# Optimization experiments

Hardware: AMD Instinct MI355X
Metric: run time of the kernel (lower is better)

Reference implementation:

```python
import jax, jax.numpy as jnp
import numpy as np
from jax import lax

C_OUT, C_IN, KH, KW = 16, 16, 3, 3
STRIDE = (1, 1)
PADDING = ((1, 1), (1, 1))  # symmetric 'same' padding for 3x3, stride 1
DILATION = (1, 1)


def setup_inputs() -> dict:
    key = jax.random.key(0)
    kx, kw = jax.random.split(key)
    x = jax.random.normal(kx, (8, C_IN, 512, 512), dtype=jnp.float32)
    # Conv2DUF stores the conv weight flattened: [out_channels, in_channels*kh*kw]
    weight = jax.random.normal(kw, (C_OUT, C_IN * KH * KW), dtype=jnp.float32) * 0.1
    return {"x": x, "weight": weight}


def reference(x, weight):
    # forward(): F.conv2d(x, weight.reshape(original shape), stride/padding/dilation/groups)
    w = weight.reshape(C_OUT, C_IN, KH, KW)
    out = lax.conv_general_dilated(
        x, w,
        window_strides=STRIDE,
        padding=PADDING,
        rhs_dilation=DILATION,
        dimension_numbers=("NCHW", "OIHW", "NCHW"),
        feature_group_count=1,
    )
    return out  # [8, 16, 512, 512]
```

## Files before the change

kernel.cpp:

```cpp
#include <hip/hip_runtime.h>
#include <hip/hip_bf16.h>


#define IH 512
#define IW 512
#define CI 16
#define CO 16

__global__ __launch_bounds__(256, 4)
void conv3x3_f32(const float* __restrict__ x, const float* __restrict__ wgt,
                 float* __restrict__ out) {
    const int t   = threadIdx.x;
    const int w0l = (t & 15) * 4;
    const int hl  = t >> 4;
    const int wb  = blockIdx.x * 64 + w0l;
    const int h   = blockIdx.y * 16 + hl;
    const int n   = blockIdx.z;

    float acc[CO][4];
#pragma unroll
    for (int co = 0; co < CO; ++co)
#pragma unroll
        for (int p = 0; p < 4; ++p) acc[co][p] = 0.0f;

    const float* xn = x + (size_t)n * CI * IH * IW;

    for (int ci = 0; ci < CI; ++ci) {
        const float* xc = xn + (size_t)ci * IH * IW;

        float r[3][6];
#pragma unroll
        for (int rr = 0; rr < 3; ++rr) {
            const int hh = h + rr - 1;
            if (hh >= 0 && hh < IH) {
                const float* p = xc + (size_t)hh * IW + wb;
                const float4 m = *(const float4*)p;
                r[rr][0] = (wb > 0)       ? p[-1] : 0.0f;
                r[rr][1] = m.x; r[rr][2] = m.y; r[rr][3] = m.z; r[rr][4] = m.w;
                r[rr][5] = (wb + 4 < IW)  ? p[4]  : 0.0f;
            } else {
#pragma unroll
                for (int j = 0; j < 6; ++j) r[rr][j] = 0.0f;
            }
        }

#pragma unroll
        for (int kh = 0; kh < 3; ++kh) {
#pragma unroll
            for (int kw = 0; kw < 3; ++kw) {
#pragma unroll
                for (int co = 0; co < CO; ++co) {
                    const float wv = wgt[co * (CI * 9) + ci * 9 + kh * 3 + kw];
#pragma unroll
                    for (int p = 0; p < 4; ++p)
                        acc[co][p] = fmaf(r[kh][kw + p], wv, acc[co][p]);
                }
            }
        }
    }

    float* on = out + (size_t)n * CO * IH * IW + (size_t)h * IW + wb;
#pragma unroll
    for (int co = 0; co < CO; ++co) {
        float4 v;
        v.x = acc[co][0]; v.y = acc[co][1]; v.z = acc[co][2]; v.w = acc[co][3];
        *(float4*)(on + (size_t)co * IH * IW) = v;
    }
}

extern "C" void kernel_launch(void* const* d_in, const int* in_sizes, int n_in,
                              void* d_out, int out_size, void* d_ws, size_t ws_size,
                              hipStream_t stream) {
    const float* x = (const float*)d_in[0];
    const float* w = (const float*)d_in[1];
    float* out     = (float*)d_out;

    dim3 grid(IW / 64, IH / 16, 8);
    dim3 block(256);
    conv3x3_f32<<<grid, block, 0, stream>>>(x, w, out);
}
```

Baseline: 301.1 us.

## Rewrite 3x3 conv as implicit GEMM on bf16 MFMA with LDS tile

Replaces the per-thread scalar FMA convolution with an implicit-GEMM formulation using 16x16x32 bf16 MFMA instructions. The input tile with halo is staged into LDS as bf16, with channels interleaved and an XOR swizzle, and the weights are preloaded as A fragments. This moves the arithmetic from scalar fp32 ALUs onto matrix cores, at the cost of bf16 rounding of both inputs and weights, which may affect accuracy against the fp32 reference.

Measured after the change: 379.4 us. +26.0%, slower.

```diff
diff --git a/kernel.cpp b/kernel.cpp
--- a/kernel.cpp
+++ b/kernel.cpp
@@ -6,65 +6,121 @@
 #define IW 512
 #define CI 16
 #define CO 16
+#define TH 16
+#define TW 64
+#define LROWS (TH + 2)
+#define LCOLS (TW + 2)
+
+typedef short short8  __attribute__((ext_vector_type(8)));
+typedef short short4v __attribute__((ext_vector_type(4)));
+typedef float f32x4   __attribute__((ext_vector_type(4)));
+
+__device__ __forceinline__ short f32_to_bf16_bits(float v) {
+    __hip_bfloat16 b = __float2bfloat16(v);
+    return __builtin_bit_cast(short, b);
+}
 
 __global__ __launch_bounds__(256, 4)
-void conv3x3_f32(const float* __restrict__ x, const float* __restrict__ wgt,
-                 float* __restrict__ out) {
-    const int t   = threadIdx.x;
-    const int w0l = (t & 15) * 4;
-    const int hl  = t >> 4;
-    const int wb  = blockIdx.x * 64 + w0l;
-    const int h   = blockIdx.y * 16 + hl;
-    const int n   = blockIdx.z;
+void conv3x3_mfma(const float* __restrict__ x, const float* __restrict__ wgt,
+                  float* __restrict__ out) {
+    __shared__ short lds[LROWS * LCOLS * CI];
 
-    float acc[CO][4];
+    const int tid  = threadIdx.x;
+    const int wave = tid >> 6;
+    const int lane = tid & 63;
+    const int quad = lane >> 4;
+    const int l15  = lane & 15;
+
+    const int wbase = blockIdx.x * TW;
+    const int hbase = blockIdx.y * TH;
+    const int n     = blockIdx.z;
+
+    short8 afrag[5];
 #pragma unroll
-    for (int co = 0; co < CO; ++co)
+    for (int f = 0; f < 5; ++f) {
 #pragma unroll
-        for (int p = 0; p < 4; ++p) acc[co][p] = 0.0f;
+        for (int j = 0; j < 8; ++j) {
+            const int k = f * 32 + quad * 8 + j;
+            float val = 0.0f;
+            if (k < 144) {
+                const int ci  = k & 15;
+                const int tap = k >> 4;
+                val = wgt[l15 * 144 + ci * 9 + tap];
+            }
+            afrag[f][j] = f32_to_bf16_bits(val);
+        }
+    }
 
     const float* xn = x + (size_t)n * CI * IH * IW;
-
-    for (int ci = 0; ci < CI; ++ci) {
-        const float* xc = xn + (size_t)ci * IH * IW;
-
-        float r[3][6];
+    for (int cg = 0; cg < CI; cg += 4) {
+        for (int row = wave; row < LROWS; row += 4) {
+            const int gh  = hbase - 1 + row;
+            const bool okh = (unsigned)gh < (unsigned)IH;
+            for (int c = lane; c < LCOLS; c += 64) {
+                const int gw = wbase - 1 + c;
+                const bool ok = okh && ((unsigned)gw < (unsigned)IW);
+                short4v pk;
 #pragma unroll
-        for (int rr = 0; rr < 3; ++rr) {
-            const int hh = h + rr - 1;
-            if (hh >= 0 && hh < IH) {
-                const float* p = xc + (size_t)hh * IW + wb;
-                const float4 m = *(const float4*)p;
-                r[rr][0] = (wb > 0)       ? p[-1] : 0.0f;
-                r[rr][1] = m.x; r[rr][2] = m.y; r[rr][3] = m.z; r[rr][4] = m.w;
-                r[rr][5] = (wb + 4 < IW)  ? p[4]  : 0.0f;
-            } else {
-#pragma unroll
-                for (int j = 0; j < 6; ++j) r[rr][j] = 0.0f;
+                for (int j = 0; j < 4; ++j) {
+                    const float v = ok ? xn[((size_t)(cg + j) * IH + gh) * IW + gw] : 0.0f;
+                    pk[j] = f32_to_bf16_bits(v);
+                }
+                const int pixel = row * LCOLS + c;
+                const int s2    = (pixel >> 1) & 2;
+                const int slot  = (cg >> 2) ^ s2;
+                *(short4v*)&lds[pixel * 16 + slot * 4] = pk;
             }
         }
+    }
+    __syncthreads();
+
+    const int q = quad & 1;
+    int doff[5];
+#pragma unroll
+    for (int f = 0; f < 5; ++f) {
+        const int tap = (f < 4) ? (f * 2 + (quad >> 1)) : 8;
+        const int kh  = tap / 3;
+        const int kw  = tap - kh * 3;
+        doff[f] = kh * LCOLS + kw;
+    }
+
+    f32x4 acc[4][4];
+#pragma unroll
+    for (int r = 0; r < 4; ++r)
+#pragma unroll
+        for (int c4 = 0; c4 < 4; ++c4)
+            acc[r][c4] = (f32x4){0.f, 0.f, 0.f, 0.f};
 
 #pragma unroll
-        for (int kh = 0; kh < 3; ++kh) {
+    for (int r = 0; r < 4; ++r) {
+        const int hl = wave * 4 + r;
 #pragma unroll
-            for (int kw = 0; kw < 3; ++kw) {
+        for (int c4 = 0; c4 < 4; ++c4) {
+            const int wl   = c4 * 16 + l15;
+            const int pbase = hl * LCOLS + wl;
 #pragma unroll
-                for (int co = 0; co < CO; ++co) {
-                    const float wv = wgt[co * (CI * 9) + ci * 9 + kh * 3 + kw];
-#pragma unroll
-                    for (int p = 0; p < 4; ++p)
-                        acc[co][p] = fmaf(r[kh][kw + p], wv, acc[co][p]);
-                }
+            for (int f = 0; f < 5; ++f) {
+                const int pixel = pbase + doff[f];
+                const int half  = q ^ ((pixel >> 2) & 1);
+                const short8 b  = *(const short8*)&lds[pixel * 16 + half * 8];
+                acc[r][c4] = __builtin_amdgcn_mfma_f32_16x16x32_bf16(afrag[f], b, acc[r][c4], 0, 0, 0);
             }
         }
     }
 
-    float* on = out + (size_t)n * CO * IH * IW + (size_t)h * IW + wb;
+    float* on = out + (size_t)n * CO * IH * IW;
 #pragma unroll
-    for (int co = 0; co < CO; ++co) {
-        float4 v;
-        v.x = acc[co][0]; v.y = acc[co][1]; v.z = acc[co][2]; v.w = acc[co][3];
-        *(float4*)(on + (size_t)co * IH * IW) = v;
+    for (int r = 0; r < 4; ++r) {
+        const int gh = hbase + wave * 4 + r;
+#pragma unroll
+        for (int c4 = 0; c4 < 4; ++c4) {
+            const int gw = wbase + c4 * 16 + l15;
+#pragma unroll
+            for (int reg = 0; reg < 4; ++reg) {
+                const int co = quad * 4 + reg;
+                on[((size_t)co * IH + gh) * IW + gw] = acc[r][c4][reg];
+            }
+        }
     }
 }
 
@@ -75,7 +131,7 @@
     const float* w = (const float*)d_in[1];
     float* out     = (float*)d_out;
 
-    dim3 grid(IW / 64, IH / 16, 8);
+    dim3 grid(IW / TW, IH / TH, 8);
     dim3 block(256);
-    conv3x3_f32<<<grid, block, 0, stream>>>(x, w, out);
+    conv3x3_mfma<<<grid, block, 0, stream>>>(x, w, out);
 }
```
